# Optimization experiments

Measured on AMD Instinct MI355X. Metric: run time of the kernel, lower is better.

Reference implementation:

```python
import jax, jax.numpy as jnp
import numpy as np

N, C, SD, A, H = 1048576, 8192, 32, 4, 64


def _xavier(key, shape):
    fan_in, fan_out = shape
    lim = np.sqrt(6.0 / (fan_in + fan_out)).astype(np.float32)
    return jax.random.uniform(key, shape, jnp.float32, -lim, lim)


def setup_inputs() -> dict:
    key = jax.random.key(0)
    ks = jax.random.split(key, 10)
    return {
        "cell_state": jax.random.normal(ks[0], (N, SD), jnp.float32),
        "arch_state": jax.random.uniform(ks[1], (N, A), jnp.float32),
        "energy": jax.random.uniform(ks[2], (N,), jnp.float32),
        "phi_local": jax.random.uniform(ks[3], (N,), jnp.float32),
        "W1": _xavier(ks[4], (SD + A, H)),
        "b1": jnp.zeros((H,), jnp.float32),
        "W2": _xavier(ks[5], (H, 1)),
        "b2": jnp.zeros((1,), jnp.float32),
        "Wc1": _xavier(ks[6], (A + 3, H // 2)),
        "bc1": jnp.zeros((H // 2,), jnp.float32),
        "Wc2": _xavier(ks[7], (H // 2, 1)),
        "bc2": jnp.zeros((1,), jnp.float32),
        "segment_ids": jnp.sort(jax.random.randint(ks[8], (N,), 0, C, jnp.int32)),
        "n_clusters": C,
    }


def reference(cell_state, arch_state, energy, phi_local,
              W1, b1, W2, b2, Wc1, bc1, Wc2, bc2,
              segment_ids, n_clusters):
    seg = segment_ids
    nc = n_clusters
    seg_sum = lambda v: jax.ops.segment_sum(v, seg, num_segments=nc)

    # ---- cells -> clusters ----
    x = jnp.concatenate([cell_state, arch_state], axis=-1)          # [N, SD+A]
    h = jax.nn.relu(x @ W1 + b1)                                    # [N, H]
    base = jax.nn.sigmoid(h @ W2 + b2)[:, 0]                        # [N]
    importance = jnp.clip(base * energy * phi_local, 0.01, 1.0)
    w = importance * energy * phi_local                              # cell weight

    counts = seg_sum(jnp.ones_like(w))                               # [C]
    wsum = seg_sum(w)                                                # [C]
    safe_cnt = jnp.maximum(counts, 1.0)
    # normalized weights; uniform fallback when a cluster's weight sum is 0
    norm_w = jnp.where(wsum[seg] > 0,
                       w / jnp.maximum(wsum, 1e-30)[seg],
                       1.0 / safe_cnt[seg])
    aggregate = seg_sum(norm_w[:, None] * arch_state)                # [C, A]

    # unbiased per-dim variance averaged over dims (torch .var(dim=0).mean())
    mean = seg_sum(arch_state) / safe_cnt[:, None]                   # [C, A]
    sqdev = seg_sum((arch_state - mean[seg]) ** 2)                   # [C, A]
    var = jnp.where(counts >= 2.0,
                    sqdev.mean(-1) / jnp.maximum(counts - 1.0, 1.0),
                    0.0)                                             # [C]
    phi_cluster = 1.0 - jnp.minimum(1.0, var * 2.0)
    coherence = 1.0 - var

    # ---- clusters -> organism ----
    feats = jnp.concatenate([aggregate,
                             phi_cluster[:, None],
                             coherence[:, None],
                             jnp.minimum(1.0, counts / 20.0)[:, None]], axis=-1)  # [C, A+3]
    hc = jax.nn.relu(feats @ Wc1 + bc1)
    basec = jax.nn.sigmoid(hc @ Wc2 + bc2)[:, 0]                     # [C]
    impc = jnp.clip(basec * phi_cluster, 0.01, 1.0)
    valid = counts > 0
    wc = jnp.where(valid, impc * counts, 0.0)
    wc_sum = wc.sum()
    nvalid = jnp.maximum(valid.sum().astype(jnp.float32), 1.0)
    norm_wc = jnp.where(wc_sum > 0,
                        wc / jnp.maximum(wc_sum, 1e-30),
                        valid.astype(jnp.float32) / nvalid)
    global_archetype = (norm_wc[:, None] * aggregate).sum(0)         # [A]

    return aggregate, phi_cluster, coherence, global_archetype
```

## Files before the change

kernel.cpp:

```cpp
#include <hip/hip_runtime.h>
#include <hip/hip_bf16.h>

#define NC 8192
#define SDIM 32
#define ADIM 4
#define XDIM 36
#define HDIM 64

typedef _Float16 half8 __attribute__((ext_vector_type(8)));
typedef float f32x4 __attribute__((ext_vector_type(4)));

__device__ __forceinline__ float sigmoidf_(float t) {
    return 1.0f / (1.0f + __expf(-t));
}

__global__ __launch_bounds__(256, 4) void mlp_kernel(
    const float* __restrict__ cell_state,
    const float* __restrict__ arch_state,
    const float* __restrict__ energy,
    const float* __restrict__ phi_local,
    const float* __restrict__ W1,
    const float* __restrict__ b1,
    const float* __restrict__ W2,
    const float* __restrict__ b2,
    const int*   __restrict__ seg,
    int* __restrict__ startx,
    int* __restrict__ endx,
    float* __restrict__ w_out,
    int n)
{
    const int tid  = threadIdx.x;
    const int lane = tid & 63;
    const int l15  = lane & 15;
    const int lg   = lane >> 4;

    {
        const int i = blockIdx.x * 256 + tid;
        if (i < n) {
            const int s = seg[i];
            if (i == 0) {
                startx[s] = 0;
                for (int c = 0; c < s; ++c) { startx[c] = 0; endx[c] = 0; }
            } else {
                const int sp = seg[i - 1];
                if (sp != s) {
                    startx[s] = i;
                    for (int c = sp + 1; c < s; ++c) { startx[c] = i; endx[c] = i; }
                }
            }
            if (i == n - 1) {
                endx[s] = n;
                for (int c = s + 1; c < NC; ++c) { startx[c] = n; endx[c] = n; }
            } else if (seg[i + 1] != s) {
                endx[s] = i + 1;
            }
        }
    }

    half8 af[4][2];
    #pragma unroll
    for (int nt = 0; nt < 4; ++nt) {
        #pragma unroll
        for (int s = 0; s < 2; ++s) {
            half8 v = {};
            #pragma unroll
            for (int jj = 0; jj < 8; ++jj) {
                const int k = 32 * s + lg * 8 + jj;
                float wv = 0.0f;
                if (k < XDIM)       wv = W1[k * HDIM + 16 * nt + l15];
                else if (k == XDIM) wv = b1[16 * nt + l15];
                v[jj] = (_Float16)wv;
            }
            af[nt][s] = v;
        }
    }
    float w2v[16];
    #pragma unroll
    for (int nt = 0; nt < 4; ++nt)
        #pragma unroll
        for (int q = 0; q < 4; ++q)
            w2v[nt * 4 + q] = W2[16 * nt + lg * 4 + q];
    const float sb2 = b2[0];

    const int chunk_base = blockIdx.x * 256 + (tid >> 6) * 64;

    float4 f0[4], f1[4];
    #pragma unroll
    for (int t = 0; t < 4; ++t) {
        int crow = chunk_base + 16 * t + l15;
        if (crow >= n) crow = n - 1;
        const float* cp = cell_state + (size_t)crow * SDIM + lg * 8;
        f0[t] = *reinterpret_cast<const float4*>(cp);
        f1[t] = *reinterpret_cast<const float4*>(cp + 4);
    }
    float4 a4[4];
    if (lg == 0) {
        #pragma unroll
        for (int t = 0; t < 4; ++t) {
            int crow = chunk_base + 16 * t + l15;
            if (crow >= n) crow = n - 1;
            a4[t] = reinterpret_cast<const float4*>(arch_state)[crow];
        }
    }
    const int gid = chunk_base + lane;
    const int lid = (gid < n) ? gid : (n - 1);
    const float e = energy[lid];
    const float p = phi_local[lid];

    float acc = 0.0f;
    #pragma unroll
    for (int t = 0; t < 4; ++t) {
        half8 x0;
        x0[0] = (_Float16)f0[t].x; x0[1] = (_Float16)f0[t].y;
        x0[2] = (_Float16)f0[t].z; x0[3] = (_Float16)f0[t].w;
        x0[4] = (_Float16)f1[t].x; x0[5] = (_Float16)f1[t].y;
        x0[6] = (_Float16)f1[t].z; x0[7] = (_Float16)f1[t].w;

        half8 x1 = {};
        if (lg == 0) {
            x1[0] = (_Float16)a4[t].x; x1[1] = (_Float16)a4[t].y;
            x1[2] = (_Float16)a4[t].z; x1[3] = (_Float16)a4[t].w;
            x1[4] = (_Float16)1.0f;
        }

        float pq = 0.0f;
        #pragma unroll
        for (int nt = 0; nt < 4; ++nt) {
            f32x4 c = f32x4{0.f, 0.f, 0.f, 0.f};
            c = __builtin_amdgcn_mfma_f32_16x16x32_f16(af[nt][0], x0, c, 0, 0, 0);
            c = __builtin_amdgcn_mfma_f32_16x16x32_f16(af[nt][1], x1, c, 0, 0, 0);
            #pragma unroll
            for (int q = 0; q < 4; ++q)
                pq = __builtin_fmaf(fmaxf(c[q], 0.0f), w2v[nt * 4 + q], pq);
        }
        pq += __shfl_xor(pq, 16);
        pq += __shfl_xor(pq, 32);
        if (lg == t) acc = pq;
    }
    const float base = sigmoidf_(acc + sb2);

    if (gid < n) {
        const float ep = e * p;
        const float imp = fminf(fmaxf(base * ep, 0.01f), 1.0f);
        w_out[gid] = imp * ep;
    }
}

__global__ __launch_bounds__(256) void cluster_kernel(
    const float* __restrict__ arch_state,
    const float* __restrict__ w_arr,
    const int*   __restrict__ startx,
    const int*   __restrict__ endx,
    const float* __restrict__ Wc1,
    const float* __restrict__ bc1,
    const float* __restrict__ Wc2,
    const float* __restrict__ bc2,
    float* __restrict__ out,
    float* __restrict__ ws2)
{
    const int lane = threadIdx.x & 63;
    const int c = blockIdx.x * 4 + (threadIdx.x >> 6);
    const int s0 = startx[c];
    const int e0 = endx[c];

    float pw = 0.0f;
    float pa0 = 0.f, pa1 = 0.f, pa2 = 0.f, pa3 = 0.f;
    float pw0 = 0.f, pw1 = 0.f, pw2 = 0.f, pw3 = 0.f;
    float pq0 = 0.f, pq1 = 0.f, pq2 = 0.f, pq3 = 0.f;
    const float4* arch4 = reinterpret_cast<const float4*>(arch_state);

    int i = s0 + lane;
    bool vcur = i < e0;
    float4 ac = {}; float wcur = 0.0f;
    if (vcur) { ac = arch4[i]; wcur = w_arr[i]; }
    while (vcur) {
        const int j = i + 64;
        const bool vnext = j < e0;
        float4 an = {}; float wnext = 0.0f;
        if (vnext) { an = arch4[j]; wnext = w_arr[j]; }
        pw += wcur;
        pa0 += ac.x; pa1 += ac.y; pa2 += ac.z; pa3 += ac.w;
        pw0 = __builtin_fmaf(wcur, ac.x, pw0); pw1 = __builtin_fmaf(wcur, ac.y, pw1);
        pw2 = __builtin_fmaf(wcur, ac.z, pw2); pw3 = __builtin_fmaf(wcur, ac.w, pw3);
        pq0 = __builtin_fmaf(ac.x, ac.x, pq0); pq1 = __builtin_fmaf(ac.y, ac.y, pq1);
        pq2 = __builtin_fmaf(ac.z, ac.z, pq2); pq3 = __builtin_fmaf(ac.w, ac.w, pq3);
        i = j; vcur = vnext; ac = an; wcur = wnext;
    }
#define RED13(F) F(pw) F(pa0) F(pa1) F(pa2) F(pa3) \
                 F(pw0) F(pw1) F(pw2) F(pw3) F(pq0) F(pq1) F(pq2) F(pq3)
#define BFLY(V) V += __shfl_xor(V, off_);
    #pragma unroll
    for (int off_ = 1; off_ < 64; off_ <<= 1) { RED13(BFLY) }

    const float cnt = (float)(e0 - s0);
    const float safe_cnt = fmaxf(cnt, 1.0f);
    const float wsum = pw;

    float agg[4];
    if (wsum > 0.0f) {
        const float inv = 1.0f / fmaxf(wsum, 1e-30f);
        agg[0] = pw0 * inv; agg[1] = pw1 * inv;
        agg[2] = pw2 * inv; agg[3] = pw3 * inv;
    } else {
        const float inv = 1.0f / safe_cnt;
        agg[0] = pa0 * inv; agg[1] = pa1 * inv;
        agg[2] = pa2 * inv; agg[3] = pa3 * inv;
    }

    const float sA[4]  = { pa0, pa1, pa2, pa3 };
    const float sA2[4] = { pq0, pq1, pq2, pq3 };
    float sq = 0.0f;
    #pragma unroll
    for (int d = 0; d < 4; ++d) {
        const float mean = sA[d] / safe_cnt;
        const float s2 = sA2[d] - 2.0f * mean * sA[d] + cnt * mean * mean;
        sq += fmaxf(s2, 0.0f);
    }
    const float var = (cnt >= 2.0f) ? (sq * 0.25f) / fmaxf(cnt - 1.0f, 1.0f) : 0.0f;
    const float phi_c = 1.0f - fminf(1.0f, var * 2.0f);
    const float coh = 1.0f - var;

    const float feats[7] = { agg[0], agg[1], agg[2], agg[3],
                             phi_c, coh, fminf(1.0f, cnt * 0.05f) };
    float t = bc2[0];
    #pragma unroll
    for (int j = 0; j < 32; ++j) {
        float hj = bc1[j];
        #pragma unroll
        for (int k = 0; k < 7; ++k)
            hj = __builtin_fmaf(feats[k], Wc1[k * 32 + j], hj);
        t += fmaxf(hj, 0.0f) * Wc2[j];
    }
    const float basec = sigmoidf_(t);
    const float impc = fminf(fmaxf(basec * phi_c, 0.01f), 1.0f);
    const bool valid = cnt > 0.0f;
    const float wc = valid ? impc * cnt : 0.0f;
    const float vf = valid ? 1.0f : 0.0f;

    if (lane == 0) {
        out[c * 4 + 0] = agg[0]; out[c * 4 + 1] = agg[1];
        out[c * 4 + 2] = agg[2]; out[c * 4 + 3] = agg[3];
        out[NC * 4 + c] = phi_c;
        out[NC * 5 + c] = coh;
        ws2[0 * NC + c] = wc;
        ws2[1 * NC + c] = vf;
        #pragma unroll
        for (int d = 0; d < 4; ++d) ws2[(2 + d) * NC + c] = wc * agg[d];
        #pragma unroll
        for (int d = 0; d < 4; ++d) ws2[(6 + d) * NC + c] = vf * agg[d];
    }
}

__global__ __launch_bounds__(1024) void finalize_kernel(
    const float* __restrict__ ws2, float* __restrict__ out)
{
    __shared__ float red[16][10];
    const int tid = threadIdx.x;
    const int lane = tid & 63;
    const int wv = tid >> 6;

    float r[10];
    #pragma unroll
    for (int k = 0; k < 10; ++k) r[k] = 0.0f;
    for (int c = tid; c < NC; c += 1024) {
        #pragma unroll
        for (int k = 0; k < 10; ++k) r[k] += ws2[k * NC + c];
    }
    #pragma unroll
    for (int off = 1; off < 64; off <<= 1) {
        #pragma unroll
        for (int k = 0; k < 10; ++k) r[k] += __shfl_xor(r[k], off);
    }
    if (lane == 0) {
        #pragma unroll
        for (int k = 0; k < 10; ++k) red[wv][k] = r[k];
    }
    __syncthreads();
    if (tid == 0) {
        float g[10];
        #pragma unroll
        for (int k = 0; k < 10; ++k) {
            float acc = 0.0f;
            for (int i = 0; i < 16; ++i) acc += red[i][k];
            g[k] = acc;
        }
        const float wcs = g[0];
        const float nv = fmaxf(g[1], 1.0f);
        #pragma unroll
        for (int d = 0; d < 4; ++d) {
            out[NC * 6 + d] = (wcs > 0.0f) ? g[2 + d] / fmaxf(wcs, 1e-30f)
                                           : g[6 + d] / nv;
        }
    }
}

extern "C" void kernel_launch(void* const* d_in, const int* in_sizes, int n_in,
                              void* d_out, int out_size, void* d_ws, size_t ws_size,
                              hipStream_t stream) {
    const float* cell_state = (const float*)d_in[0];
    const float* arch_state = (const float*)d_in[1];
    const float* energy     = (const float*)d_in[2];
    const float* phi_local  = (const float*)d_in[3];
    const float* W1  = (const float*)d_in[4];
    const float* b1  = (const float*)d_in[5];
    const float* W2  = (const float*)d_in[6];
    const float* b2  = (const float*)d_in[7];
    const float* Wc1 = (const float*)d_in[8];
    const float* bc1 = (const float*)d_in[9];
    const float* Wc2 = (const float*)d_in[10];
    const float* bc2 = (const float*)d_in[11];
    const int* seg   = (const int*)d_in[12];

    const int n = in_sizes[2];
    float* out = (float*)d_out;

    float* w_arr = (float*)d_ws;
    int* startx  = (int*)(w_arr + n);
    int* endx    = startx + NC;
    float* ws2   = (float*)(endx + NC);

    const int nb = (n + 255) / 256;
    mlp_kernel<<<nb, 256, 0, stream>>>(cell_state, arch_state, energy, phi_local,
                                       W1, b1, W2, b2, seg, startx, endx, w_arr, n);
    cluster_kernel<<<NC / 4, 256, 0, stream>>>(arch_state, w_arr, startx, endx,
                                               Wc1, bc1, Wc2, bc2, out, ws2);
    finalize_kernel<<<1, 1024, 0, stream>>>(ws2, out);
}
```

Measured before the change: 76.72 us.

## Make MLP kernel persistent with software-pipelined prefetch of next chunk

The MLP kernel now launches a fixed grid of 1024 blocks instead of one block per 256 cells. Each wave walks over 64-row chunks in a grid-stride loop and issues the global loads for the next chunk before running the MFMA work on the current one. The segment-boundary scan is also turned into a grid-stride loop. The aim is to hide memory latency and cut the fixed cost of weight setup per block. The trade-off is extra registers for the prefetched data, which may lower occupancy.

```diff
diff --git a/kernel.cpp b/kernel.cpp
--- a/kernel.cpp
+++ b/kernel.cpp
@@ -9,6 +9,8 @@
 
 typedef _Float16 half8 __attribute__((ext_vector_type(8)));
 typedef float f32x4 __attribute__((ext_vector_type(4)));
+
+#define MLP_BLOCKS 1024
 
 __device__ __forceinline__ float sigmoidf_(float t) {
     return 1.0f / (1.0f + __expf(-t));
@@ -34,26 +36,23 @@
     const int l15  = lane & 15;
     const int lg   = lane >> 4;
 
-    {
-        const int i = blockIdx.x * 256 + tid;
-        if (i < n) {
-            const int s = seg[i];
-            if (i == 0) {
-                startx[s] = 0;
-                for (int c = 0; c < s; ++c) { startx[c] = 0; endx[c] = 0; }
-            } else {
-                const int sp = seg[i - 1];
-                if (sp != s) {
-                    startx[s] = i;
-                    for (int c = sp + 1; c < s; ++c) { startx[c] = i; endx[c] = i; }
-                }
+    for (int i = blockIdx.x * 256 + tid; i < n; i += gridDim.x * 256) {
+        const int s = seg[i];
+        if (i == 0) {
+            startx[s] = 0;
+            for (int c = 0; c < s; ++c) { startx[c] = 0; endx[c] = 0; }
+        } else {
+            const int sp = seg[i - 1];
+            if (sp != s) {
+                startx[s] = i;
+                for (int c = sp + 1; c < s; ++c) { startx[c] = i; endx[c] = i; }
             }
-            if (i == n - 1) {
-                endx[s] = n;
-                for (int c = s + 1; c < NC; ++c) { startx[c] = n; endx[c] = n; }
-            } else if (seg[i + 1] != s) {
-                endx[s] = i + 1;
-            }
+        }
+        if (i == n - 1) {
+            endx[s] = n;
+            for (int c = s + 1; c < NC; ++c) { startx[c] = n; endx[c] = n; }
+        } else if (seg[i + 1] != s) {
+            endx[s] = i + 1;
         }
     }
 
@@ -82,68 +81,91 @@
             w2v[nt * 4 + q] = W2[16 * nt + lg * 4 + q];
     const float sb2 = b2[0];
 
-    const int chunk_base = blockIdx.x * 256 + (tid >> 6) * 64;
-
-    float4 f0[4], f1[4];
-    #pragma unroll
-    for (int t = 0; t < 4; ++t) {
-        int crow = chunk_base + 16 * t + l15;
-        if (crow >= n) crow = n - 1;
-        const float* cp = cell_state + (size_t)crow * SDIM + lg * 8;
-        f0[t] = *reinterpret_cast<const float4*>(cp);
-        f1[t] = *reinterpret_cast<const float4*>(cp + 4);
-    }
-    float4 a4[4];
-    if (lg == 0) {
+    const int nch = (n + 63) >> 6;
+    const int wid = blockIdx.x * 4 + (tid >> 6);
+    const int nw  = gridDim.x * 4;
+
+    float4 f0[4], f1[4], a4[4];
+    float e = 0.f, p = 0.f;
+
+#define ISSUE_LOADS(C)                                                        \
+    {                                                                         \
+        const int base_ = (C) * 64;                                           \
+        _Pragma("unroll")                                                     \
+        for (int t = 0; t < 4; ++t) {                                         \
+            int crow = base_ + 16 * t + l15;                                  \
+            if (crow >= n) crow = n - 1;                                      \
+            const float* cp = cell_state + (size_t)crow * SDIM + lg * 8;      \
+            f0[t] = *reinterpret_cast<const float4*>(cp);                     \
+            f1[t] = *reinterpret_cast<const float4*>(cp + 4);                 \
+        }                                                                     \
+        if (lg == 0) {                                                        \
+            _Pragma("unroll")                                                 \
+            for (int t = 0; t < 4; ++t) {                                     \
+                int crow = base_ + 16 * t + l15;                              \
+                if (crow >= n) crow = n - 1;                                  \
+                a4[t] = reinterpret_cast<const float4*>(arch_state)[crow];    \
+            }                                                                 \
+        }                                                                     \
+        int gid_ = base_ + lane; if (gid_ >= n) gid_ = n - 1;                 \
+        e = energy[gid_]; p = phi_local[gid_];                                \
+    }
+
+    int c = wid;
+    if (c < nch) ISSUE_LOADS(c);
+
+    #pragma unroll 1
+    while (c < nch) {
+        half8 x0[4], x1[4];
         #pragma unroll
         for (int t = 0; t < 4; ++t) {
-            int crow = chunk_base + 16 * t + l15;
-            if (crow >= n) crow = n - 1;
-            a4[t] = reinterpret_cast<const float4*>(arch_state)[crow];
-        }
-    }
-    const int gid = chunk_base + lane;
-    const int lid = (gid < n) ? gid : (n - 1);
-    const float e = energy[lid];
-    const float p = phi_local[lid];
-
-    float acc = 0.0f;
-    #pragma unroll
-    for (int t = 0; t < 4; ++t) {
-        half8 x0;
-        x0[0] = (_Float16)f0[t].x; x0[1] = (_Float16)f0[t].y;
-        x0[2] = (_Float16)f0[t].z; x0[3] = (_Float16)f0[t].w;
-        x0[4] = (_Float16)f1[t].x; x0[5] = (_Float16)f1[t].y;
-        x0[6] = (_Float16)f1[t].z; x0[7] = (_Float16)f1[t].w;
-
-        half8 x1 = {};
-        if (lg == 0) {
-            x1[0] = (_Float16)a4[t].x; x1[1] = (_Float16)a4[t].y;
-            x1[2] = (_Float16)a4[t].z; x1[3] = (_Float16)a4[t].w;
-            x1[4] = (_Float16)1.0f;
-        }
-
-        float pq = 0.0f;
-        #pragma unroll
-        for (int nt = 0; nt < 4; ++nt) {
-            f32x4 c = f32x4{0.f, 0.f, 0.f, 0.f};
-            c = __builtin_amdgcn_mfma_f32_16x16x32_f16(af[nt][0], x0, c, 0, 0, 0);
-            c = __builtin_amdgcn_mfma_f32_16x16x32_f16(af[nt][1], x1, c, 0, 0, 0);
+            half8 v;
+            v[0] = (_Float16)f0[t].x; v[1] = (_Float16)f0[t].y;
+            v[2] = (_Float16)f0[t].z; v[3] = (_Float16)f0[t].w;
+            v[4] = (_Float16)f1[t].x; v[5] = (_Float16)f1[t].y;
+            v[6] = (_Float16)f1[t].z; v[7] = (_Float16)f1[t].w;
+            x0[t] = v;
+            half8 u = {};
+            if (lg == 0) {
+                u[0] = (_Float16)a4[t].x; u[1] = (_Float16)a4[t].y;
+                u[2] = (_Float16)a4[t].z; u[3] = (_Float16)a4[t].w;
+                u[4] = (_Float16)1.0f;
+            }
+            x1[t] = u;
+        }
+        const float ecur = e, pcur = p;
+        const int ccur = c;
+
+        c += nw;
+        if (c < nch) ISSUE_LOADS(c);
+
+        float acc = 0.0f;
+        #pragma unroll
+        for (int t = 0; t < 4; ++t) {
+            float pq = 0.0f;
             #pragma unroll
-            for (int q = 0; q < 4; ++q)
-                pq = __builtin_fmaf(fmaxf(c[q], 0.0f), w2v[nt * 4 + q], pq);
-        }
-        pq += __shfl_xor(pq, 16);
-        pq += __shfl_xor(pq, 32);
-        if (lg == t) acc = pq;
-    }
-    const float base = sigmoidf_(acc + sb2);
-
-    if (gid < n) {
-        const float ep = e * p;
-        const float imp = fminf(fmaxf(base * ep, 0.01f), 1.0f);
-        w_out[gid] = imp * ep;
-    }
+            for (int nt = 0; nt < 4; ++nt) {
+                f32x4 cc = f32x4{0.f, 0.f, 0.f, 0.f};
+                cc = __builtin_amdgcn_mfma_f32_16x16x32_f16(af[nt][0], x0[t], cc, 0, 0, 0);
+                cc = __builtin_amdgcn_mfma_f32_16x16x32_f16(af[nt][1], x1[t], cc, 0, 0, 0);
+                #pragma unroll
+                for (int q = 0; q < 4; ++q)
+                    pq = __builtin_fmaf(fmaxf(cc[q], 0.0f), w2v[nt * 4 + q], pq);
+            }
+            pq += __shfl_xor(pq, 16);
+            pq += __shfl_xor(pq, 32);
+            if (lg == t) acc = pq;
+        }
+        const float base = sigmoidf_(acc + sb2);
+
+        const int gid = ccur * 64 + lane;
+        if (gid < n) {
+            const float ep = ecur * pcur;
+            const float imp = fminf(fmaxf(base * ep, 0.01f), 1.0f);
+            w_out[gid] = imp * ep;
+        }
+    }
+#undef ISSUE_LOADS
 }
 
 __global__ __launch_bounds__(256) void cluster_kernel(
@@ -319,9 +341,9 @@
     int* endx    = startx + NC;
     float* ws2   = (float*)(endx + NC);
 
-    const int nb = (n + 255) / 256;
-    mlp_kernel<<<nb, 256, 0, stream>>>(cell_state, arch_state, energy, phi_local,
-                                       W1, b1, W2, b2, seg, startx, endx, w_arr, n);
+    mlp_kernel<<<MLP_BLOCKS, 256, 0, stream>>>(cell_state, arch_state, energy,
+                                               phi_local, W1, b1, W2, b2, seg,
+                                               startx, endx, w_arr, n);
     cluster_kernel<<<NC / 4, 256, 0, stream>>>(arch_state, w_arr, startx, endx,
                                                Wc1, bc1, Wc2, bc2, out, ws2);
     finalize_kernel<<<1, 1024, 0, stream>>>(ws2, out);
```

After: 115.8 us. +50.9%, slower.

## Make MLP kernel persistent with grid-stride chunks and LDS-staged W1 fragments

Applied to the files above, without the earlier changes.

The MLP kernel now launches a fixed 1024 blocks and gives each wave a contiguous range of 64-row chunks instead of one block per 256 rows. W1/b1 are packed into fp16 MFMA fragments once per block by one wave, staged through shared memory, and reused across all chunks. This cuts the per-block cost of rebuilding weight fragments and the number of blocks launched. In exchange the loop runs with unroll 1, which loses overlap of loads across chunks, and fewer waves are in flight to hide memory latency.

```diff
diff --git a/kernel.cpp b/kernel.cpp
--- a/kernel.cpp
+++ b/kernel.cpp
@@ -6,6 +6,7 @@
 #define ADIM 4
 #define XDIM 36
 #define HDIM 64
+#define MLP_BLOCKS 1024
 
 typedef _Float16 half8 __attribute__((ext_vector_type(8)));
 typedef float f32x4 __attribute__((ext_vector_type(4)));
@@ -29,51 +30,61 @@
     float* __restrict__ w_out,
     int n)
 {
+    __shared__ half8 wpack[8 * 64];
     const int tid  = threadIdx.x;
     const int lane = tid & 63;
     const int l15  = lane & 15;
     const int lg   = lane >> 4;
 
-    {
-        const int i = blockIdx.x * 256 + tid;
-        if (i < n) {
-            const int s = seg[i];
-            if (i == 0) {
-                startx[s] = 0;
-                for (int c = 0; c < s; ++c) { startx[c] = 0; endx[c] = 0; }
-            } else {
-                const int sp = seg[i - 1];
-                if (sp != s) {
-                    startx[s] = i;
-                    for (int c = sp + 1; c < s; ++c) { startx[c] = i; endx[c] = i; }
+    for (int i = blockIdx.x * 256 + tid; i < n; i += gridDim.x * 256) {
+        const int s = seg[i];
+        if (i == 0) {
+            startx[s] = 0;
+            for (int c = 0; c < s; ++c) { startx[c] = 0; endx[c] = 0; }
+        } else {
+            const int sp = seg[i - 1];
+            if (sp != s) {
+                startx[s] = i;
+                for (int c = sp + 1; c < s; ++c) { startx[c] = i; endx[c] = i; }
+            }
+        }
+        if (i == n - 1) {
+            endx[s] = n;
+            for (int c = s + 1; c < NC; ++c) { startx[c] = n; endx[c] = n; }
+        } else if (seg[i + 1] != s) {
+            endx[s] = i + 1;
+        }
+    }
+
+    if (tid < 64) {
+        const int pl15 = tid & 15;
+        const int plg  = tid >> 4;
+        #pragma unroll
+        for (int nt = 0; nt < 4; ++nt) {
+            #pragma unroll
+            for (int s = 0; s < 2; ++s) {
+                half8 v = {};
+                #pragma unroll
+                for (int jj = 0; jj < 8; ++jj) {
+                    const int k = 32 * s + plg * 8 + jj;
+                    float wv = 0.0f;
+                    if (k < XDIM)       wv = W1[k * HDIM + 16 * nt + pl15];
+                    else if (k == XDIM) wv = b1[16 * nt + pl15];
+                    v[jj] = (_Float16)wv;
                 }
-            }
-            if (i == n - 1) {
-                endx[s] = n;
-                for (int c = s + 1; c < NC; ++c) { startx[c] = n; endx[c] = n; }
-            } else if (seg[i + 1] != s) {
-                endx[s] = i + 1;
-            }
-        }
-    }
+                wpack[(nt * 2 + s) * 64 + tid] = v;
+            }
+        }
+    }
+    __syncthreads();
 
     half8 af[4][2];
     #pragma unroll
-    for (int nt = 0; nt < 4; ++nt) {
-        #pragma unroll
-        for (int s = 0; s < 2; ++s) {
-            half8 v = {};
-            #pragma unroll
-            for (int jj = 0; jj < 8; ++jj) {
-                const int k = 32 * s + lg * 8 + jj;
-                float wv = 0.0f;
-                if (k < XDIM)       wv = W1[k * HDIM + 16 * nt + l15];
-                else if (k == XDIM) wv = b1[16 * nt + l15];
-                v[jj] = (_Float16)wv;
-            }
-            af[nt][s] = v;
-        }
-    }
+    for (int nt = 0; nt < 4; ++nt)
+        #pragma unroll
+        for (int s = 0; s < 2; ++s)
+            af[nt][s] = wpack[(nt * 2 + s) * 64 + lane];
+
     float w2v[16];
     #pragma unroll
     for (int nt = 0; nt < 4; ++nt)
@@ -82,67 +93,77 @@
             w2v[nt * 4 + q] = W2[16 * nt + lg * 4 + q];
     const float sb2 = b2[0];
 
-    const int chunk_base = blockIdx.x * 256 + (tid >> 6) * 64;
-
-    float4 f0[4], f1[4];
-    #pragma unroll
-    for (int t = 0; t < 4; ++t) {
-        int crow = chunk_base + 16 * t + l15;
-        if (crow >= n) crow = n - 1;
-        const float* cp = cell_state + (size_t)crow * SDIM + lg * 8;
-        f0[t] = *reinterpret_cast<const float4*>(cp);
-        f1[t] = *reinterpret_cast<const float4*>(cp + 4);
-    }
-    float4 a4[4];
-    if (lg == 0) {
+    const int nch = (n + 63) >> 6;
+    const int nw  = gridDim.x * 4;
+    const int wid = blockIdx.x * 4 + (tid >> 6);
+    const int chw = (nch + nw - 1) / nw;
+
+    #pragma unroll 1
+    for (int j = 0; j < chw; ++j) {
+        const int c = wid * chw + j;
+        if (c >= nch) break;
+        const int chunk_base = c * 64;
+
+        float4 f0[4], f1[4];
         #pragma unroll
         for (int t = 0; t < 4; ++t) {
             int crow = chunk_base + 16 * t + l15;
             if (crow >= n) crow = n - 1;
-            a4[t] = reinterpret_cast<const float4*>(arch_state)[crow];
-        }
-    }
-    const int gid = chunk_base + lane;
-    const int lid = (gid < n) ? gid : (n - 1);
-    const float e = energy[lid];
-    const float p = phi_local[lid];
-
-    float acc = 0.0f;
-    #pragma unroll
-    for (int t = 0; t < 4; ++t) {
-        half8 x0;
-        x0[0] = (_Float16)f0[t].x; x0[1] = (_Float16)f0[t].y;
-        x0[2] = (_Float16)f0[t].z; x0[3] = (_Float16)f0[t].w;
-        x0[4] = (_Float16)f1[t].x; x0[5] = (_Float16)f1[t].y;
-        x0[6] = (_Float16)f1[t].z; x0[7] = (_Float16)f1[t].w;
-
-        half8 x1 = {};
+            const float* cp = cell_state + (size_t)crow * SDIM + lg * 8;
+            f0[t] = *reinterpret_cast<const float4*>(cp);
+            f1[t] = *reinterpret_cast<const float4*>(cp + 4);
+        }
+        float4 a4[4];
         if (lg == 0) {
-            x1[0] = (_Float16)a4[t].x; x1[1] = (_Float16)a4[t].y;
-            x1[2] = (_Float16)a4[t].z; x1[3] = (_Float16)a4[t].w;
-            x1[4] = (_Float16)1.0f;
-        }
-
-        float pq = 0.0f;
-        #pragma unroll
-        for (int nt = 0; nt < 4; ++nt) {
-            f32x4 c = f32x4{0.f, 0.f, 0.f, 0.f};
-            c = __builtin_amdgcn_mfma_f32_16x16x32_f16(af[nt][0], x0, c, 0, 0, 0);
-            c = __builtin_amdgcn_mfma_f32_16x16x32_f16(af[nt][1], x1, c, 0, 0, 0);
             #pragma unroll
-            for (int q = 0; q < 4; ++q)
-                pq = __builtin_fmaf(fmaxf(c[q], 0.0f), w2v[nt * 4 + q], pq);
-        }
-        pq += __shfl_xor(pq, 16);
-        pq += __shfl_xor(pq, 32);
-        if (lg == t) acc = pq;
-    }
-    const float base = sigmoidf_(acc + sb2);
-
-    if (gid < n) {
-        const float ep = e * p;
-        const float imp = fminf(fmaxf(base * ep, 0.01f), 1.0f);
-        w_out[gid] = imp * ep;
+            for (int t = 0; t < 4; ++t) {
+                int crow = chunk_base + 16 * t + l15;
+                if (crow >= n) crow = n - 1;
+                a4[t] = reinterpret_cast<const float4*>(arch_state)[crow];
+            }
+        }
+        const int gid = chunk_base + lane;
+        const int lid = (gid < n) ? gid : (n - 1);
+        const float e = energy[lid];
+        const float p = phi_local[lid];
+
+        float acc = 0.0f;
+        #pragma unroll
+        for (int t = 0; t < 4; ++t) {
+            half8 x0;
+            x0[0] = (_Float16)f0[t].x; x0[1] = (_Float16)f0[t].y;
+            x0[2] = (_Float16)f0[t].z; x0[3] = (_Float16)f0[t].w;
+            x0[4] = (_Float16)f1[t].x; x0[5] = (_Float16)f1[t].y;
+            x0[6] = (_Float16)f1[t].z; x0[7] = (_Float16)f1[t].w;
+
+            half8 x1 = {};
+            if (lg == 0) {
+                x1[0] = (_Float16)a4[t].x; x1[1] = (_Float16)a4[t].y;
+                x1[2] = (_Float16)a4[t].z; x1[3] = (_Float16)a4[t].w;
+                x1[4] = (_Float16)1.0f;
+            }
+
+            float pq = 0.0f;
+            #pragma unroll
+            for (int nt = 0; nt < 4; ++nt) {
+                f32x4 cc = f32x4{0.f, 0.f, 0.f, 0.f};
+                cc = __builtin_amdgcn_mfma_f32_16x16x32_f16(af[nt][0], x0, cc, 0, 0, 0);
+                cc = __builtin_amdgcn_mfma_f32_16x16x32_f16(af[nt][1], x1, cc, 0, 0, 0);
+                #pragma unroll
+                for (int q = 0; q < 4; ++q)
+                    pq = __builtin_fmaf(fmaxf(cc[q], 0.0f), w2v[nt * 4 + q], pq);
+            }
+            pq += __shfl_xor(pq, 16);
+            pq += __shfl_xor(pq, 32);
+            if (lg == t) acc = pq;
+        }
+        const float base = sigmoidf_(acc + sb2);
+
+        if (gid < n) {
+            const float ep = e * p;
+            const float imp = fminf(fmaxf(base * ep, 0.01f), 1.0f);
+            w_out[gid] = imp * ep;
+        }
     }
 }
 
@@ -319,9 +340,9 @@
     int* endx    = startx + NC;
     float* ws2   = (float*)(endx + NC);
 
-    const int nb = (n + 255) / 256;
-    mlp_kernel<<<nb, 256, 0, stream>>>(cell_state, arch_state, energy, phi_local,
-                                       W1, b1, W2, b2, seg, startx, endx, w_arr, n);
+    mlp_kernel<<<MLP_BLOCKS, 256, 0, stream>>>(cell_state, arch_state, energy,
+                                               phi_local, W1, b1, W2, b2, seg,
+                                               startx, endx, w_arr, n);
     cluster_kernel<<<NC / 4, 256, 0, stream>>>(arch_state, w_arr, startx, endx,
                                                Wc1, bc1, Wc2, bc2, out, ws2);
     finalize_kernel<<<1, 1024, 0, stream>>>(ws2, out);
```

After: 64.96 us. 1.18x faster.
